# Kernel tuning notes

Measured on AMD Instinct MI355X. Metric: run time of the kernel, lower is better.

Reference implementation:

```python
import jax, jax.numpy as jnp
import numpy as np

QUANT_BLOCK = 32  # hardcoded in Linear8Bit


def setup_inputs() -> dict:
    key = jax.random.key(0)
    k1, k2, k3, k4, k5 = jax.random.split(key, 5)
    M, K, N = 64, 8192, 8192
    num_blocks = K // QUANT_BLOCK  # 256
    x = jax.random.normal(k1, (M, K), dtype=jnp.float32)
    scales = jax.random.uniform(k2, (num_blocks, N), dtype=jnp.float32, minval=0.001, maxval=0.02)
    zeros = jax.random.uniform(k3, (num_blocks, N), dtype=jnp.float32, minval=0.0, maxval=255.0)
    bias = jax.random.normal(k4, (N,), dtype=jnp.float32)
    quantized_weight = jax.random.randint(k5, (K, N), 0, 256, dtype=jnp.int32)
    return {"x": x, "scales": scales, "zeros": zeros, "bias": bias,
            "quantized_weight": quantized_weight}


def reference(x, scales, zeros, bias, quantized_weight):
    # The torch loop computes sum_b a_block @ (scale_b * (w_block - zero_b)),
    # which is exactly a full block-wise dequant followed by one matmul.
    K, N = quantized_weight.shape
    # Expand per-block scale/zero along K: [num_blocks, N] -> [K, N]
    scale_k = jnp.repeat(scales, QUANT_BLOCK, axis=0)[:K]
    zero_k = jnp.repeat(zeros, QUANT_BLOCK, axis=0)[:K]
    w_dq = scale_k * (quantized_weight.astype(jnp.float32) - zero_k)  # [K, N]
    out = jnp.matmul(x, w_dq) + bias  # [M, N]
    return out
```

## Files before the change

### kernel.cpp

```cpp
#include <hip/hip_runtime.h>

#define M_DIM 64
#define K_DIM 8192
#define N_DIM 8192
#define QB 32
#define NT 64
#define KC 64
#define SPLITS 4
#define KSPLIT (K_DIM / SPLITS)
#define NSTAGE (KSPLIT / KC)

typedef __attribute__((ext_vector_type(8))) short short8;
typedef __attribute__((ext_vector_type(8))) unsigned short ushort8;
typedef __attribute__((ext_vector_type(4))) float f32x4;

static_assert(NSTAGE * KC == KSPLIT, "split must tile");

__device__ __forceinline__ unsigned short f2bf(float f) {
    unsigned u = __builtin_bit_cast(unsigned, f);
    u += 0x7fffu + ((u >> 16) & 1u);
    return (unsigned short)(u >> 16);
}

__global__ __launch_bounds__(256) void bias_init(const float* __restrict__ bias,
                                                 float* __restrict__ out) {
    int i = (blockIdx.x * 256 + threadIdx.x) * 4;
    *(f32x4*)(out + i) = *(const f32x4*)(bias + (i & (N_DIM - 1)));
}

template <bool PART>
__global__ __launch_bounds__(256, 2) void qgemm(
    const float* __restrict__ x,
    const float* __restrict__ scales,
    const float* __restrict__ zeros,
    const int*   __restrict__ qw,
    float*       __restrict__ outp)
{
    __shared__ unsigned short lq[2][NT][72];
    __shared__ unsigned short lx[2][M_DIM][72];

    const int tid  = threadIdx.x;
    const int lane = tid & 63;
    const int w    = tid >> 6;

    const int n0 = blockIdx.x * NT;
    const int k0 = blockIdx.y * KSPLIT;

    const int qn   = n0 + lane;
    const int xrow = tid >> 2;
    const int xcol = (tid & 3) * 16;

    int   qv[16];
    float sv0, sv1, zv0, zv1;
    f32x4 xv[4];

    auto load_stage = [&](int kk) {
        #pragma unroll
        for (int s = 0; s < 4; ++s)
            #pragma unroll
            for (int j = 0; j < 4; ++j)
                qv[s * 4 + j] = qw[(size_t)(kk + 16 * s + 4 * w + j) * N_DIM + qn];
        const int b0 = kk >> 5;
        sv0 = scales[(size_t)b0 * N_DIM + qn];
        sv1 = scales[(size_t)(b0 + 1) * N_DIM + qn];
        zv0 = zeros[(size_t)b0 * N_DIM + qn];
        zv1 = zeros[(size_t)(b0 + 1) * N_DIM + qn];
        #pragma unroll
        for (int i = 0; i < 4; ++i)
            xv[i] = *(const f32x4*)(x + (size_t)xrow * K_DIM + kk + xcol + 4 * i);
    };

    load_stage(k0);

    f32x4 acc[4];
    #pragma unroll
    for (int r = 0; r < 4; ++r) acc[r] = (f32x4){0.f, 0.f, 0.f, 0.f};

    for (int t = 0; t < NSTAGE; ++t) {
        const int cur = t & 1;

        const float nz0 = -sv0 * zv0, nz1 = -sv1 * zv1;
        const float s0r = sv0, s1r = sv1;
        uint2 qd[4];
        #pragma unroll
        for (int s = 0; s < 4; ++s) {
            const float sc = (s < 2) ? s0r : s1r;
            const float nz = (s < 2) ? nz0 : nz1;
            unsigned short h0 = f2bf(fmaf((float)qv[s * 4 + 0], sc, nz));
            unsigned short h1 = f2bf(fmaf((float)qv[s * 4 + 1], sc, nz));
            unsigned short h2 = f2bf(fmaf((float)qv[s * 4 + 2], sc, nz));
            unsigned short h3 = f2bf(fmaf((float)qv[s * 4 + 3], sc, nz));
            qd[s].x = (unsigned)h0 | ((unsigned)h1 << 16);
            qd[s].y = (unsigned)h2 | ((unsigned)h3 << 16);
        }
        ushort8 xw0, xw1;
        #pragma unroll
        for (int e = 0; e < 4; ++e) {
            xw0[e]     = f2bf(xv[0][e]);
            xw0[4 + e] = f2bf(xv[1][e]);
            xw1[e]     = f2bf(xv[2][e]);
            xw1[4 + e] = f2bf(xv[3][e]);
        }

        if (t + 1 < NSTAGE) load_stage(k0 + (t + 1) * KC);

        #pragma unroll
        for (int s = 0; s < 4; ++s)
            *(uint2*)&lq[cur][lane][16 * s + 4 * w] = qd[s];
        *(ushort8*)&lx[cur][xrow][xcol]     = xw0;
        *(ushort8*)&lx[cur][xrow][xcol + 8] = xw1;

        __syncthreads();

        #pragma unroll
        for (int c = 0; c < 2; ++c) {
            const short8 bf = *(const short8*)&lq[cur][16 * w + (lane & 15)]
                                                [32 * c + 8 * (lane >> 4)];
            #pragma unroll
            for (int r = 0; r < 4; ++r) {
                const short8 af = *(const short8*)&lx[cur][16 * r + (lane & 15)]
                                                    [32 * c + 8 * (lane >> 4)];
                acc[r] = __builtin_amdgcn_mfma_f32_16x16x32_bf16(af, bf, acc[r], 0, 0, 0);
            }
        }
    }

    const int cn = n0 + 16 * w + (lane & 15);
    if (PART) {
        float* po = outp + (size_t)blockIdx.y * (M_DIM * (size_t)N_DIM);
        #pragma unroll
        for (int r = 0; r < 4; ++r) {
            const int m = 16 * r + 4 * (lane >> 4);
            #pragma unroll
            for (int e = 0; e < 4; ++e)
                po[(size_t)(m + e) * N_DIM + cn] = acc[r][e];
        }
    } else {
        #pragma unroll
        for (int r = 0; r < 4; ++r) {
            const int m = 16 * r + 4 * (lane >> 4);
            #pragma unroll
            for (int e = 0; e < 4; ++e)
                atomicAdd(outp + (size_t)(m + e) * N_DIM + cn, acc[r][e]);
        }
    }
}

__global__ __launch_bounds__(256) void reduce_bias(const float* __restrict__ part,
                                                   const float* __restrict__ bias,
                                                   float* __restrict__ out) {
    int i = (blockIdx.x * 256 + threadIdx.x) * 4;
    f32x4 s = *(const f32x4*)(bias + (i & (N_DIM - 1)));
    #pragma unroll
    for (int sp = 0; sp < SPLITS; ++sp)
        s += *(const f32x4*)(part + (size_t)sp * (M_DIM * (size_t)N_DIM) + i);
    *(f32x4*)(out + i) = s;
}

extern "C" void kernel_launch(void* const* d_in, const int* in_sizes, int n_in,
                              void* d_out, int out_size, void* d_ws, size_t ws_size,
                              hipStream_t stream) {
    const float* x      = (const float*)d_in[0];
    const float* scales = (const float*)d_in[1];
    const float* zeros  = (const float*)d_in[2];
    const float* bias   = (const float*)d_in[3];
    const int*   qw     = (const int*)d_in[4];
    float* out  = (float*)d_out;
    float* part = (float*)d_ws;

    const size_t need = (size_t)SPLITS * M_DIM * N_DIM * sizeof(float);

    if (ws_size >= need) {
        qgemm<true><<<dim3(N_DIM / NT, SPLITS), 256, 0, stream>>>(
            x, scales, zeros, qw, part);
        reduce_bias<<<dim3((M_DIM * N_DIM) / 1024), 256, 0, stream>>>(part, bias, out);
    } else {
        bias_init<<<dim3((M_DIM * N_DIM) / 1024), 256, 0, stream>>>(bias, out);
        qgemm<false><<<dim3(N_DIM / NT, SPLITS), 256, 0, stream>>>(
            x, scales, zeros, qw, out);
    }
}
```

Baseline: 59.36 us.

## Widen N tile to 128 with 2-wide weight loads and double split-K

Each block now covers 128 output columns. Each thread loads int2/float2 pairs of weights, scales and zeros, and each wave computes two 16-column MFMA groups that share the same x fragment. Split-K goes from 4 to 8 so the grid stays the same size. This halves redundant x staging and conversion per column and widens global loads, but doubles the partial-sum buffer traffic in the reduce kernel and raises register pressure. The LDS lq array is still declared [NT] rows and is now written at 128 rows.

After: 63.34 us. +6.7%, slower.

```diff
diff --git a/kernel.cpp b/kernel.cpp
--- a/kernel.cpp
+++ b/kernel.cpp
@@ -4,9 +4,9 @@
 #define K_DIM 8192
 #define N_DIM 8192
 #define QB 32
-#define NT 64
+#define NT 128
 #define KC 64
-#define SPLITS 4
+#define SPLITS 8
 #define KSPLIT (K_DIM / SPLITS)
 #define NSTAGE (KSPLIT / KC)
 
@@ -42,29 +42,32 @@
     const int tid  = threadIdx.x;
     const int lane = tid & 63;
     const int w    = tid >> 6;
+    const int q    = lane >> 4;
+    const int lm   = lane & 15;
 
     const int n0 = blockIdx.x * NT;
     const int k0 = blockIdx.y * KSPLIT;
 
-    const int qn   = n0 + lane;
+    const int cp   = n0 + 2 * lane;
     const int xrow = tid >> 2;
     const int xcol = (tid & 3) * 16;
 
-    int   qv[16];
-    float sv0, sv1, zv0, zv1;
-    f32x4 xv[4];
+    int2   qv[16];
+    float2 sv[2], zv[2];
+    f32x4  xv[4];
 
     auto load_stage = [&](int kk) {
         #pragma unroll
         for (int s = 0; s < 4; ++s)
             #pragma unroll
             for (int j = 0; j < 4; ++j)
-                qv[s * 4 + j] = qw[(size_t)(kk + 16 * s + 4 * w + j) * N_DIM + qn];
+                qv[4 * s + j] = *(const int2*)(qw +
+                    (size_t)(kk + 16 * s + 4 * w + j) * N_DIM + cp);
         const int b0 = kk >> 5;
-        sv0 = scales[(size_t)b0 * N_DIM + qn];
-        sv1 = scales[(size_t)(b0 + 1) * N_DIM + qn];
-        zv0 = zeros[(size_t)b0 * N_DIM + qn];
-        zv1 = zeros[(size_t)(b0 + 1) * N_DIM + qn];
+        sv[0] = *(const float2*)(scales + (size_t)b0 * N_DIM + cp);
+        sv[1] = *(const float2*)(scales + (size_t)(b0 + 1) * N_DIM + cp);
+        zv[0] = *(const float2*)(zeros  + (size_t)b0 * N_DIM + cp);
+        zv[1] = *(const float2*)(zeros  + (size_t)(b0 + 1) * N_DIM + cp);
         #pragma unroll
         for (int i = 0; i < 4; ++i)
             xv[i] = *(const f32x4*)(x + (size_t)xrow * K_DIM + kk + xcol + 4 * i);
@@ -72,26 +75,35 @@
 
     load_stage(k0);
 
-    f32x4 acc[4];
+    f32x4 acc[2][4];
     #pragma unroll
-    for (int r = 0; r < 4; ++r) acc[r] = (f32x4){0.f, 0.f, 0.f, 0.f};
+    for (int g = 0; g < 2; ++g)
+        #pragma unroll
+        for (int r = 0; r < 4; ++r) acc[g][r] = (f32x4){0.f, 0.f, 0.f, 0.f};
 
     for (int t = 0; t < NSTAGE; ++t) {
         const int cur = t & 1;
 
-        const float nz0 = -sv0 * zv0, nz1 = -sv1 * zv1;
-        const float s0r = sv0, s1r = sv1;
-        uint2 qd[4];
+        const float2 nz0 = {-sv[0].x * zv[0].x, -sv[0].y * zv[0].y};
+        const float2 nz1 = {-sv[1].x * zv[1].x, -sv[1].y * zv[1].y};
+        const float2 s0r = sv[0], s1r = sv[1];
+        uint2 qd0[4], qd1[4];
         #pragma unroll
         for (int s = 0; s < 4; ++s) {
-            const float sc = (s < 2) ? s0r : s1r;
-            const float nz = (s < 2) ? nz0 : nz1;
-            unsigned short h0 = f2bf(fmaf((float)qv[s * 4 + 0], sc, nz));
-            unsigned short h1 = f2bf(fmaf((float)qv[s * 4 + 1], sc, nz));
-            unsigned short h2 = f2bf(fmaf((float)qv[s * 4 + 2], sc, nz));
-            unsigned short h3 = f2bf(fmaf((float)qv[s * 4 + 3], sc, nz));
-            qd[s].x = (unsigned)h0 | ((unsigned)h1 << 16);
-            qd[s].y = (unsigned)h2 | ((unsigned)h3 << 16);
+            const float2 sc = (s < 2) ? s0r : s1r;
+            const float2 nz = (s < 2) ? nz0 : nz1;
+            unsigned short a0 = f2bf(fmaf((float)qv[4 * s + 0].x, sc.x, nz.x));
+            unsigned short a1 = f2bf(fmaf((float)qv[4 * s + 1].x, sc.x, nz.x));
+            unsigned short a2 = f2bf(fmaf((float)qv[4 * s + 2].x, sc.x, nz.x));
+            unsigned short a3 = f2bf(fmaf((float)qv[4 * s + 3].x, sc.x, nz.x));
+            unsigned short b0 = f2bf(fmaf((float)qv[4 * s + 0].y, sc.y, nz.y));
+            unsigned short b1 = f2bf(fmaf((float)qv[4 * s + 1].y, sc.y, nz.y));
+            unsigned short b2 = f2bf(fmaf((float)qv[4 * s + 2].y, sc.y, nz.y));
+            unsigned short b3 = f2bf(fmaf((float)qv[4 * s + 3].y, sc.y, nz.y));
+            qd0[s].x = (unsigned)a0 | ((unsigned)a1 << 16);
+            qd0[s].y = (unsigned)a2 | ((unsigned)a3 << 16);
+            qd1[s].x = (unsigned)b0 | ((unsigned)b1 << 16);
+            qd1[s].y = (unsigned)b2 | ((unsigned)b3 << 16);
         }
         ushort8 xw0, xw1;
         #pragma unroll
@@ -105,8 +117,10 @@
         if (t + 1 < NSTAGE) load_stage(k0 + (t + 1) * KC);
 
         #pragma unroll
-        for (int s = 0; s < 4; ++s)
-            *(uint2*)&lq[cur][lane][16 * s + 4 * w] = qd[s];
+        for (int s = 0; s < 4; ++s) {
+            *(uint2*)&lq[cur][2 * lane][16 * s + 4 * w]     = qd0[s];
+            *(uint2*)&lq[cur][2 * lane + 1][16 * s + 4 * w] = qd1[s];
+        }
         *(ushort8*)&lx[cur][xrow][xcol]     = xw0;
         *(ushort8*)&lx[cur][xrow][xcol + 8] = xw1;
 
@@ -114,34 +128,41 @@
 
         #pragma unroll
         for (int c = 0; c < 2; ++c) {
-            const short8 bf = *(const short8*)&lq[cur][16 * w + (lane & 15)]
-                                                [32 * c + 8 * (lane >> 4)];
+            short8 bf[2];
+            #pragma unroll
+            for (int g = 0; g < 2; ++g)
+                bf[g] = *(const short8*)&lq[cur][32 * w + 16 * g + lm][32 * c + 8 * q];
             #pragma unroll
             for (int r = 0; r < 4; ++r) {
-                const short8 af = *(const short8*)&lx[cur][16 * r + (lane & 15)]
-                                                    [32 * c + 8 * (lane >> 4)];
-                acc[r] = __builtin_amdgcn_mfma_f32_16x16x32_bf16(af, bf, acc[r], 0, 0, 0);
+                const short8 af = *(const short8*)&lx[cur][16 * r + lm][32 * c + 8 * q];
+                #pragma unroll
+                for (int g = 0; g < 2; ++g)
+                    acc[g][r] = __builtin_amdgcn_mfma_f32_16x16x32_bf16(
+                        af, bf[g], acc[g][r], 0, 0, 0);
             }
         }
     }
 
-    const int cn = n0 + 16 * w + (lane & 15);
-    if (PART) {
-        float* po = outp + (size_t)blockIdx.y * (M_DIM * (size_t)N_DIM);
-        #pragma unroll
-        for (int r = 0; r < 4; ++r) {
-            const int m = 16 * r + 4 * (lane >> 4);
-            #pragma unroll
-            for (int e = 0; e < 4; ++e)
-                po[(size_t)(m + e) * N_DIM + cn] = acc[r][e];
-        }
-    } else {
-        #pragma unroll
-        for (int r = 0; r < 4; ++r) {
-            const int m = 16 * r + 4 * (lane >> 4);
-            #pragma unroll
-            for (int e = 0; e < 4; ++e)
-                atomicAdd(outp + (size_t)(m + e) * N_DIM + cn, acc[r][e]);
+    #pragma unroll
+    for (int g = 0; g < 2; ++g) {
+        const int cn = n0 + 32 * w + 16 * g + lm;
+        if (PART) {
+            float* po = outp + (size_t)blockIdx.y * (M_DIM * (size_t)N_DIM);
+            #pragma unroll
+            for (int r = 0; r < 4; ++r) {
+                const int m = 16 * r + 4 * q;
+                #pragma unroll
+                for (int e = 0; e < 4; ++e)
+                    po[(size_t)(m + e) * N_DIM + cn] = acc[g][r][e];
+            }
+        } else {
+            #pragma unroll
+            for (int r = 0; r < 4; ++r) {
+                const int m = 16 * r + 4 * q;
+                #pragma unroll
+                for (int e = 0; e < 4; ++e)
+                    atomicAdd(outp + (size_t)(m + e) * N_DIM + cn, acc[g][r][e]);
+            }
         }
     }
 }
```

## Pre-convert x to bf16, remap block order, use nontemporal weight loads

Applied to the files above, without the earlier changes.

Adds a separate kernel that converts x to bf16 once into workspace, so the GEMM blocks load half as many activation bytes and skip the per-stage float-to-bf16 conversion. Flattens the grid and remaps block indices so consecutive blocks cover neighbouring N tiles across K-splits, which may change cache and XCD locality. Streams the weights, scales and zeros with nontemporal loads to avoid polluting cache. This costs an extra kernel launch and a larger workspace requirement.

New measurement: 65.18 us. 9.8% more time.

```diff
diff --git a/kernel.cpp b/kernel.cpp
--- a/kernel.cpp
+++ b/kernel.cpp
@@ -13,6 +13,7 @@
 typedef __attribute__((ext_vector_type(8))) short short8;
 typedef __attribute__((ext_vector_type(8))) unsigned short ushort8;
 typedef __attribute__((ext_vector_type(4))) float f32x4;
+typedef __attribute__((ext_vector_type(4))) unsigned int u32x4;
 
 static_assert(NSTAGE * KC == KSPLIT, "split must tile");
 
@@ -28,9 +29,21 @@
     *(f32x4*)(out + i) = *(const f32x4*)(bias + (i & (N_DIM - 1)));
 }
 
-template <bool PART>
+__global__ __launch_bounds__(256) void xcvt(const float* __restrict__ x,
+                                            unsigned short* __restrict__ xb) {
+    int i = (blockIdx.x * 256 + threadIdx.x) * 8;
+    f32x4 a = *(const f32x4*)(x + i);
+    f32x4 b = *(const f32x4*)(x + i + 4);
+    ushort8 o;
+    #pragma unroll
+    for (int e = 0; e < 4; ++e) { o[e] = f2bf(a[e]); o[4 + e] = f2bf(b[e]); }
+    *(ushort8*)(xb + i) = o;
+}
+
+template <bool XBF, bool PART>
 __global__ __launch_bounds__(256, 2) void qgemm(
     const float* __restrict__ x,
+    const unsigned short* __restrict__ xb,
     const float* __restrict__ scales,
     const float* __restrict__ zeros,
     const int*   __restrict__ qw,
@@ -43,8 +56,12 @@
     const int lane = tid & 63;
     const int w    = tid >> 6;
 
-    const int n0 = blockIdx.x * NT;
-    const int k0 = blockIdx.y * KSPLIT;
+    const int L  = blockIdx.x;
+    const int by = (L & 7) >> 1;
+    const int bx = (L >> 3) * 2 + (L & 1);
+
+    const int n0 = bx * NT;
+    const int k0 = by * KSPLIT;
 
     const int qn   = n0 + lane;
     const int xrow = tid >> 2;
@@ -52,22 +69,30 @@
 
     int   qv[16];
     float sv0, sv1, zv0, zv1;
-    f32x4 xv[4];
+    u32x4 xv[2];
+    f32x4 xf[4];
 
     auto load_stage = [&](int kk) {
         #pragma unroll
         for (int s = 0; s < 4; ++s)
             #pragma unroll
             for (int j = 0; j < 4; ++j)
-                qv[s * 4 + j] = qw[(size_t)(kk + 16 * s + 4 * w + j) * N_DIM + qn];
+                qv[s * 4 + j] = __builtin_nontemporal_load(
+                    qw + (size_t)(kk + 16 * s + 4 * w + j) * N_DIM + qn);
         const int b0 = kk >> 5;
-        sv0 = scales[(size_t)b0 * N_DIM + qn];
-        sv1 = scales[(size_t)(b0 + 1) * N_DIM + qn];
-        zv0 = zeros[(size_t)b0 * N_DIM + qn];
-        zv1 = zeros[(size_t)(b0 + 1) * N_DIM + qn];
-        #pragma unroll
-        for (int i = 0; i < 4; ++i)
-            xv[i] = *(const f32x4*)(x + (size_t)xrow * K_DIM + kk + xcol + 4 * i);
+        sv0 = __builtin_nontemporal_load(scales + (size_t)b0 * N_DIM + qn);
+        sv1 = __builtin_nontemporal_load(scales + (size_t)(b0 + 1) * N_DIM + qn);
+        zv0 = __builtin_nontemporal_load(zeros  + (size_t)b0 * N_DIM + qn);
+        zv1 = __builtin_nontemporal_load(zeros  + (size_t)(b0 + 1) * N_DIM + qn);
+        if (XBF) {
+            const unsigned short* xp = xb + (size_t)xrow * K_DIM + kk + xcol;
+            xv[0] = *(const u32x4*)xp;
+            xv[1] = *(const u32x4*)(xp + 8);
+        } else {
+            const float* xp = x + (size_t)xrow * K_DIM + kk + xcol;
+            #pragma unroll
+            for (int i = 0; i < 4; ++i) xf[i] = *(const f32x4*)(xp + 4 * i);
+        }
     };
 
     load_stage(k0);
@@ -93,13 +118,21 @@
             qd[s].x = (unsigned)h0 | ((unsigned)h1 << 16);
             qd[s].y = (unsigned)h2 | ((unsigned)h3 << 16);
         }
-        ushort8 xw0, xw1;
-        #pragma unroll
-        for (int e = 0; e < 4; ++e) {
-            xw0[e]     = f2bf(xv[0][e]);
-            xw0[4 + e] = f2bf(xv[1][e]);
-            xw1[e]     = f2bf(xv[2][e]);
-            xw1[4 + e] = f2bf(xv[3][e]);
+        u32x4 xw0, xw1;
+        if (XBF) {
+            xw0 = xv[0];
+            xw1 = xv[1];
+        } else {
+            ushort8 a, b;
+            #pragma unroll
+            for (int e = 0; e < 4; ++e) {
+                a[e]     = f2bf(xf[0][e]);
+                a[4 + e] = f2bf(xf[1][e]);
+                b[e]     = f2bf(xf[2][e]);
+                b[4 + e] = f2bf(xf[3][e]);
+            }
+            xw0 = __builtin_bit_cast(u32x4, a);
+            xw1 = __builtin_bit_cast(u32x4, b);
         }
 
         if (t + 1 < NSTAGE) load_stage(k0 + (t + 1) * KC);
@@ -107,8 +140,8 @@
         #pragma unroll
         for (int s = 0; s < 4; ++s)
             *(uint2*)&lq[cur][lane][16 * s + 4 * w] = qd[s];
-        *(ushort8*)&lx[cur][xrow][xcol]     = xw0;
-        *(ushort8*)&lx[cur][xrow][xcol + 8] = xw1;
+        *(u32x4*)&lx[cur][xrow][xcol]     = xw0;
+        *(u32x4*)&lx[cur][xrow][xcol + 8] = xw1;
 
         __syncthreads();
 
@@ -127,7 +160,7 @@
 
     const int cn = n0 + 16 * w + (lane & 15);
     if (PART) {
-        float* po = outp + (size_t)blockIdx.y * (M_DIM * (size_t)N_DIM);
+        float* po = outp + (size_t)by * (M_DIM * (size_t)N_DIM);
         #pragma unroll
         for (int r = 0; r < 4; ++r) {
             const int m = 16 * r + 4 * (lane >> 4);
@@ -165,18 +198,20 @@
     const float* zeros  = (const float*)d_in[2];
     const float* bias   = (const float*)d_in[3];
     const int*   qw     = (const int*)d_in[4];
-    float* out  = (float*)d_out;
-    float* part = (float*)d_ws;
-
-    const size_t need = (size_t)SPLITS * M_DIM * N_DIM * sizeof(float);
+    float* out = (float*)d_out;
+
+    unsigned short* xbf = (unsigned short*)d_ws;
+    float* part = (float*)((char*)d_ws + (2u << 20));
+    const size_t need = (2u << 20) + (size_t)SPLITS * M_DIM * N_DIM * sizeof(float);
 
     if (ws_size >= need) {
-        qgemm<true><<<dim3(N_DIM / NT, SPLITS), 256, 0, stream>>>(
-            x, scales, zeros, qw, part);
+        xcvt<<<dim3((M_DIM * K_DIM) / 2048), 256, 0, stream>>>(x, xbf);
+        qgemm<true, true><<<dim3((N_DIM / NT) * SPLITS), 256, 0, stream>>>(
+            x, xbf, scales, zeros, qw, part);
         reduce_bias<<<dim3((M_DIM * N_DIM) / 1024), 256, 0, stream>>>(part, bias, out);
     } else {
         bias_init<<<dim3((M_DIM * N_DIM) / 1024), 256, 0, stream>>>(bias, out);
-        qgemm<false><<<dim3(N_DIM / NT, SPLITS), 256, 0, stream>>>(
-            x, scales, zeros, qw, out);
+        qgemm<false, false><<<dim3((N_DIM / NT) * SPLITS), 256, 0, stream>>>(
+            x, nullptr, scales, zeros, qw, out);
     }
 }
```
